# Performance work log

Hardware: AMD Instinct MI355X
Metric: run time of the kernel (lower is better)

The kernel has to match this reference:

```python
import jax, jax.numpy as jnp
import numpy as np

B, T, S, D, V, L = 32, 128, 256, 1024, 10000, 2
EOS = 2


def setup_inputs() -> dict:
    key = jax.random.key(0)
    ks = jax.random.split(key, 12)
    s = 0.02
    targets = jax.random.randint(ks[0], (B, T), 0, V)
    targets = jnp.where(targets == EOS, 3, targets)  # decoder strips eos; keep rectangular
    return {
        'encoder_outputs': jax.random.normal(ks[1], (B, S, D), jnp.float32),
        'targets': targets,
        'emb': jax.random.normal(ks[2], (V, D)) * s,
        'W_ih': jax.random.normal(ks[3], (L, 4 * D, D)) * s,
        'W_hh': jax.random.normal(ks[4], (L, 4 * D, D)) * s,
        'b_ih': jnp.zeros((L, 4 * D)),
        'b_hh': jnp.zeros((L, 4 * D)),
        'Wconv': jax.random.normal(ks[5], (D, 3)) * s,   # Conv1d(1 -> attn_dim, k=3) kernel
        'bconv': jnp.zeros((D,)),
        'Wq': jax.random.normal(ks[6], (D, D)) * s,      # query_proj (no bias)
        'Wv': jax.random.normal(ks[7], (D, D)) * s,      # value_proj (no bias)
        'attn_bias': jax.random.uniform(ks[8], (D,), minval=-0.1, maxval=0.1),
        'fc_attn_w': jax.random.normal(ks[9], (D,)) * s, # attention score fc (D -> 1)
        'fc_attn_b': jnp.zeros(()),
        'fc1_w': jax.random.normal(ks[10], (D, 2 * D)) * s,  # Linear(2D -> D)
        'fc1_b': jnp.zeros((D,)),
        'fc2_w': jax.random.normal(ks[11], (V, D)) * s,      # Linear(D -> V)
        'fc2_b': jnp.zeros((V,)),
    }


def _forward(encoder_outputs, targets, emb, W_ih, W_hh, b_ih, b_hh, Wconv, bconv,
             Wq, Wv, attn_bias, fc_attn_w, fc_attn_b, fc1_w, fc1_b, fc2_w, fc2_b):
    b, s_len = encoder_outputs.shape[0], encoder_outputs.shape[1]
    # value_proj(encoder_outputs) is constant across decode steps
    vproj = jnp.einsum('bsd,ed->bse', encoder_outputs, Wv)
    embedded = emb[targets]                  # (B,T,D)
    xs = jnp.swapaxes(embedded, 0, 1)        # (T,B,D)
    h0 = jnp.zeros((L, b, D), embedded.dtype)
    c0 = jnp.zeros((L, b, D), embedded.dtype)
    a0 = jnp.zeros((b, s_len), embedded.dtype)  # last alignment energy starts at zero

    def step(carry, x_t):
        h, c, attn = carry
        inp = x_t
        hs, cs = [], []
        for l in range(L):  # fixed small number of LSTM layers
            gates = inp @ W_ih[l].T + b_ih[l] + h[l] @ W_hh[l].T + b_hh[l]
            i, f, g, o = jnp.split(gates, 4, axis=-1)
            c_l = jax.nn.sigmoid(f) * c[l] + jax.nn.sigmoid(i) * jnp.tanh(g)
            h_l = jax.nn.sigmoid(o) * jnp.tanh(c_l)
            hs.append(h_l); cs.append(c_l); inp = h_l
        q = inp  # decoder rnn output for this step, (B,D)
        # location_conv: Conv1d(1->D, k=3, pad=1) over last alignment
        pad = jnp.pad(attn, ((0, 0), (1, 1)))
        win = jnp.stack([pad[:, :-2], pad[:, 1:-1], pad[:, 2:]], axis=-1)  # (B,S,3)
        loc = jnp.einsum('bsk,dk->bsd', win, Wconv) + bconv
        qp = q @ Wq.T
        e = jnp.tanh(qp[:, None, :] + vproj + loc + attn_bias)  # (B,S,D)
        energy = jnp.einsum('bsd,d->bs', e, fc_attn_w) + fc_attn_b
        new_attn = jax.nn.softmax(energy, axis=-1)
        context = jnp.einsum('bs,bsd->bd', new_attn, encoder_outputs)
        hid = jnp.tanh(jnp.concatenate([q, context], axis=-1) @ fc1_w.T + fc1_b)
        logp = jax.nn.log_softmax(hid @ fc2_w.T + fc2_b, axis=-1)
        return (jnp.stack(hs), jnp.stack(cs), new_attn), logp

    _, logps = jax.lax.scan(step, (h0, c0, a0), xs)  # (T,B,V)
    return jnp.swapaxes(logps, 0, 1)                 # (B,T,V) log-probs


def reference(encoder_outputs, targets, emb, W_ih, W_hh, b_ih, b_hh, Wconv, bconv,
              Wq, Wv, attn_bias, fc_attn_w, fc_attn_b, fc1_w, fc1_b, fc2_w, fc2_b):
    return _forward(encoder_outputs, targets, emb, W_ih, W_hh, b_ih, b_hh, Wconv, bconv,
                    Wq, Wv, attn_bias, fc_attn_w, fc_attn_b, fc1_w, fc1_b, fc2_w, fc2_b)
```

## Files before the change

kernel.cpp:

```cpp
#include <hip/hip_runtime.h>
#include <stdint.h>

#define B_ 32
#define T_ 128
#define S_ 256
#define D_ 1024
#define V_ 10000

typedef unsigned short u16;
typedef unsigned long long u64;
typedef __attribute__((ext_vector_type(8))) short bf16x8;
typedef __attribute__((ext_vector_type(4))) float f32x4;

__device__ __forceinline__ float bf2f(u16 u){ union { unsigned int i; float f; } v; v.i = ((unsigned int)u)<<16; return v.f; }
__device__ __forceinline__ u16 f2bf(float f){ union { float ff; unsigned int i; } v; v.ff = f; unsigned int x = v.i; return (u16)((x + 0x7fffu + ((x>>16)&1u))>>16); }
__device__ __forceinline__ float ftanh(float x){
  float e = __expf(2.f*x);
  return __builtin_fmaf(-2.f, __builtin_amdgcn_rcpf(1.f+e), 1.f);
}
__device__ __forceinline__ float sigm(float x){
  return __builtin_amdgcn_rcpf(1.f + __expf(-x));
}

__global__ void k_cast(const float* __restrict__ in, u16* __restrict__ out, long n){
  for (long i = (long)blockIdx.x*blockDim.x + threadIdx.x; i < n; i += (long)gridDim.x*blockDim.x)
    out[i] = f2bf(in[i]);
}

__global__ void k_w1cat(const float* __restrict__ wih1, const float* __restrict__ whh1, u16* __restrict__ out){
  const long n = (long)4096*2048;
  for (long i = (long)blockIdx.x*blockDim.x + threadIdx.x; i < n; i += (long)gridDim.x*blockDim.x){
    int row = (int)(i >> 11), k = (int)(i & 2047);
    float v = (k < D_) ? wih1[(size_t)row*D_ + k] : whh1[(size_t)row*D_ + (k - D_)];
    out[i] = f2bf(v);
  }
}

__global__ void k_bias(const float* __restrict__ bih, const float* __restrict__ bhh,
                       const float* __restrict__ bcv, const float* __restrict__ abias,
                       const float* __restrict__ Wcv, const float* __restrict__ fcw,
                       float* __restrict__ bias0, float* __restrict__ bias1,
                       float* __restrict__ biasE, float* __restrict__ convw){
  int i = blockIdx.x*blockDim.x + threadIdx.x;
  if (i < 4096){ bias0[i] = bih[i]+bhh[i]; bias1[i] = bih[4096+i]+bhh[4096+i]; }
  if (i < 1024){
    biasE[i] = bcv[i]+abias[i];
    convw[i*4+0]=Wcv[i*3+0]; convw[i*4+1]=Wcv[i*3+1]; convw[i*4+2]=Wcv[i*3+2]; convw[i*4+3]=fcw[i];
  }
}

__global__ void k_gather(const float* __restrict__ emb, const int* __restrict__ tgt, u16* __restrict__ embA){
  int row = blockIdx.x;
  int t = row >> 5, b = row & 31;
  int e = tgt[b*T_ + t];
  const float* src = emb + (size_t)e*D_;
  u16* dst = embA + (size_t)row*D_;
  for (int d = threadIdx.x; d < D_; d += 256) dst[d] = f2bf(src[d]);
}

__device__ __forceinline__ void gld_lds(const u16* g, u16* l){
  __builtin_amdgcn_global_load_lds((const __attribute__((address_space(1))) unsigned int*)g,
                                   (__attribute__((address_space(3))) unsigned int*)l, 16, 0, 0);
}

template<int OUT_MODE, bool SWIZ>
__global__ __launch_bounds__(256) void k_gemm128(const u16* __restrict__ Am, const u16* __restrict__ Bm,
      const float* __restrict__ bias, void* __restrict__ Cout, int M, int N, int K, int lda, int ldc)
{
  __shared__ u16 As[128*32];
  __shared__ u16 Bs[128*32];
  int bm = blockIdx.y*128, bn = blockIdx.x*128;
  int tid = threadIdx.x;
  int wv = tid>>6, lane = tid&63;
  int wm = (wv>>1)*64, wn = (wv&1)*64;
  int r = lane&15, kh = lane>>4;
  f32x4 zero = {0.f,0.f,0.f,0.f};
  f32x4 acc[4][4];
  #pragma unroll
  for (int mi=0;mi<4;mi++)
    #pragma unroll
    for (int ni=0;ni<4;ni++) acc[mi][ni] = zero;

  for (int k0 = 0; k0 < K; k0 += 32){
    #pragma unroll
    for (int i=0;i<2;i++){
      int c = tid + i*256;
      int row = c>>2, ko = (c&3)*8;
      int ga = bm+row; if (ga > M-1) ga = M-1;
      gld_lds(Am + (size_t)ga*lda + k0 + ko, As + c*8);
      int gb = bn+row; if (gb > N-1) gb = N-1;
      gld_lds(Bm + (size_t)gb*K + k0 + ko, Bs + c*8);
    }
    __syncthreads();
    bf16x8 af[4], bfv[4];
    #pragma unroll
    for (int mi=0;mi<4;mi++) af[mi]  = *(const bf16x8*)(As + (wm+mi*16+r)*32 + kh*8);
    #pragma unroll
    for (int ni=0;ni<4;ni++) bfv[ni] = *(const bf16x8*)(Bs + (wn+ni*16+r)*32 + kh*8);
    #pragma unroll
    for (int mi=0;mi<4;mi++)
      #pragma unroll
      for (int ni=0;ni<4;ni++)
        acc[mi][ni] = __builtin_amdgcn_mfma_f32_16x16x32_bf16(af[mi], bfv[ni], acc[mi][ni], 0,0,0);
    __syncthreads();
  }
  #pragma unroll
  for (int mi=0;mi<4;mi++)
    #pragma unroll
    for (int ni=0;ni<4;ni++)
      #pragma unroll
      for (int rr=0;rr<4;rr++){
        int grow = bm+wm+mi*16+kh*4+rr;
        int gcol = bn+wn+ni*16+r;
        if (grow < M && gcol < N){
          float v = acc[mi][ni][rr];
          if (bias) v += bias[gcol];
          size_t orow = SWIZ ? (size_t)((grow&31)*T_ + (grow>>5)) : (size_t)grow;
          if (OUT_MODE==0)      ((float*)Cout)[orow*(size_t)ldc + gcol] = v;
          else if (OUT_MODE==1) ((u16*)Cout)[orow*(size_t)ldc + gcol] = f2bf(v);
          else                  ((u16*)Cout)[orow*(size_t)ldc + gcol] = f2bf(ftanh(v));
        }
      }
}

__device__ __forceinline__ void xcd_barrier(int* barL, int it){
  asm volatile("s_waitcnt vmcnt(0)" ::: "memory");
  __syncthreads();
  if (threadIdx.x==0){
    int grp = blockIdx.x & 7;
    int* gcnt = barL + grp*32;
    int* root = barL + 256;
    int* rel  = barL + 320 + grp*32;
    int v = __hip_atomic_fetch_add(gcnt, 1, __ATOMIC_RELAXED, __HIP_MEMORY_SCOPE_AGENT);
    if (v == 32*(it+1) - 1){
      int rv = __hip_atomic_fetch_add(root, 1, __ATOMIC_RELAXED, __HIP_MEMORY_SCOPE_AGENT);
      if (rv == 8*(it+1) - 1){
        #pragma unroll
        for (int g2=0; g2<8; ++g2)
          __hip_atomic_store(barL + 320 + g2*32, it+1, __ATOMIC_RELAXED, __HIP_MEMORY_SCOPE_AGENT);
      }
    }
    while (__hip_atomic_load(rel, __ATOMIC_RELAXED, __HIP_MEMORY_SCOPE_AGENT) < it+1)
      __builtin_amdgcn_s_sleep(8);
  }
  __syncthreads();
}

__device__ __forceinline__ void ring_barrier(int* cnt, int nblk, int it){
  asm volatile("s_waitcnt vmcnt(0)" ::: "memory");
  __syncthreads();
  if (threadIdx.x==0){
    __hip_atomic_fetch_add(cnt, 1, __ATOMIC_RELAXED, __HIP_MEMORY_SCOPE_AGENT);
    int target = nblk*(it+1);
    while (__hip_atomic_load(cnt, __ATOMIC_RELAXED, __HIP_MEMORY_SCOPE_AGENT) < target)
      __builtin_amdgcn_s_sleep(4);
  }
  __syncthreads();
}

__global__ __launch_bounds__(512) void k_lstm_p(const u16* __restrict__ Whh0, const u16* __restrict__ W1cat,
    const u16* __restrict__ X0, const float* __restrict__ bias1,
    u16* __restrict__ Hh, u16* __restrict__ qcat, int* __restrict__ barL)
{
  __shared__ u16 W0s[16*1024];
  __shared__ u16 W1s[16*2048];
  __shared__ float gl0[8*512];
  __shared__ float gl1[8*512];
  __shared__ u16 hb0[128];
  __shared__ u16 hb1[128];
  int bid = blockIdx.x, tid = threadIdx.x;
  int w = tid>>6, lane = tid&63, r = lane&15, kh = lane>>4;
  for (int ci = tid; ci < 2048; ci += 512){
    int row = ci>>7, c = ci&127;
    int grow = (row>>2)*1024 + bid*4 + (row&3);
    bf16x8 v = *(const bf16x8*)(Whh0 + (size_t)grow*1024 + c*8);
    *(bf16x8*)(W0s + (size_t)(((row<<7) + (c ^ (row&7)))*8)) = v;
  }
  for (int ci = tid; ci < 4096; ci += 512){
    int row = ci>>8, c = ci&255;
    int grow = (row>>2)*1024 + bid*4 + (row&3);
    bf16x8 v = *(const bf16x8*)(W1cat + (size_t)grow*2048 + c*8);
    *(bf16x8*)(W1s + (size_t)(((row<<8) + (c ^ (row&7)))*8)) = v;
  }
  __syncthreads();
  float c0reg = 0.f, c1reg = 0.f;
  int cb = tid>>2, cj = tid&3;
  int col = bid*4 + cj;
  float b1i=0.f, b1f=0.f, b1g=0.f, b1o=0.f;
  if (tid < 128){ b1i=bias1[col]; b1f=bias1[1024+col]; b1g=bias1[2048+col]; b1o=bias1[3072+col]; }
  for (int p = 0; p <= T_; ++p){
    const u16* Hprev = Hh + (size_t)p*65536;
    u16* Hcur = (u16*)Hh + (size_t)(p+1)*65536;
    bool doG0 = (p < T_), doG1 = (p > 0);
    float x_gi=0.f, x_gf=0.f, x_gg=0.f, x_go=0.f;
    if (doG0 && tid < 128){
      const u16* xr = X0 + ((size_t)p*32 + cb)*4096 + col;
      x_gi = bf2f(xr[0]); x_gf = bf2f(xr[1024]); x_gg = bf2f(xr[2048]); x_go = bf2f(xr[3072]);
    }
    f32x4 acc00={0.f,0.f,0.f,0.f}, acc01={0.f,0.f,0.f,0.f};
    f32x4 acc10={0.f,0.f,0.f,0.f}, acc11={0.f,0.f,0.f,0.f};
    bf16x8 a_g0[2][4], a_g1[2][8];
    if (doG0){
      const u16* a0 = Hprev + (size_t)r*2048 + w*128 + kh*8;
      const u16* a1 = Hprev + (size_t)(16+r)*2048 + w*128 + kh*8;
      #pragma unroll
      for (int kk=0;kk<4;kk++){ a_g0[0][kk] = *(const bf16x8*)(a0 + kk*32);
                                a_g0[1][kk] = *(const bf16x8*)(a1 + kk*32); }
    }
    if (doG1){
      const u16* a0 = Hprev + (size_t)r*2048 + w*256 + kh*8;
      const u16* a1 = Hprev + (size_t)(16+r)*2048 + w*256 + kh*8;
      #pragma unroll
      for (int kk=0;kk<8;kk++){ a_g1[0][kk] = *(const bf16x8*)(a0 + kk*32);
                                a_g1[1][kk] = *(const bf16x8*)(a1 + kk*32); }
    }
    if (doG0){
      #pragma unroll
      for (int kk=0;kk<4;kk++){
        int c = (w<<4) + (kk<<2) + kh;
        bf16x8 bv = *(const bf16x8*)(W0s + (size_t)((((int)r<<7) + (c ^ (r&7)))*8));
        acc00 = __builtin_amdgcn_mfma_f32_16x16x32_bf16(a_g0[0][kk], bv, acc00, 0,0,0);
        acc01 = __builtin_amdgcn_mfma_f32_16x16x32_bf16(a_g0[1][kk], bv, acc01, 0,0,0);
      }
    }
    if (doG1){
      #pragma unroll
      for (int kk=0;kk<8;kk++){
        int c = (w<<5) + (kk<<2) + kh;
        bf16x8 bv = *(const bf16x8*)(W1s + (size_t)((((int)r<<8) + (c ^ (r&7)))*8));
        acc10 = __builtin_amdgcn_mfma_f32_16x16x32_bf16(a_g1[0][kk], bv, acc10, 0,0,0);
        acc11 = __builtin_amdgcn_mfma_f32_16x16x32_bf16(a_g1[1][kk], bv, acc11, 0,0,0);
      }
    }
    #pragma unroll
    for (int rr=0;rr<4;rr++){
      gl0[w*512 + (kh*4+rr)*16 + r]    = acc00[rr];
      gl0[w*512 + (16+kh*4+rr)*16 + r] = acc01[rr];
      gl1[w*512 + (kh*4+rr)*16 + r]    = acc10[rr];
      gl1[w*512 + (16+kh*4+rr)*16 + r] = acc11[rr];
    }
    __syncthreads();
    if (tid < 128){
      if (doG0){
        float gi=x_gi, gf=x_gf, gg=x_gg, go=x_go;
        #pragma unroll
        for (int ww=0;ww<8;ww++){
          const float* gp = gl0 + ww*512 + cb*16 + cj;
          gi += gp[0]; gf += gp[4]; gg += gp[8]; go += gp[12];
        }
        float cn = sigm(gf)*c0reg + sigm(gi)*ftanh(gg);
        float hn = sigm(go)*ftanh(cn); c0reg = cn;
        hb0[tid] = f2bf(hn);
      }
      if (doG1){
        float gi=b1i, gf=b1f, gg=b1g, go=b1o;
        #pragma unroll
        for (int ww=0;ww<8;ww++){
          const float* gp = gl1 + ww*512 + cb*16 + cj;
          gi += gp[0]; gf += gp[4]; gg += gp[8]; go += gp[12];
        }
        float cn = sigm(gf)*c1reg + sigm(gi)*ftanh(gg);
        float hn = sigm(go)*ftanh(cn); c1reg = cn;
        hb1[tid] = f2bf(hn);
      }
    }
    __syncthreads();
    if (tid < 32){
      union { u64 v; u16 s[4]; } pk;
      if (doG0){
        pk.s[0]=hb0[tid*4]; pk.s[1]=hb0[tid*4+1]; pk.s[2]=hb0[tid*4+2]; pk.s[3]=hb0[tid*4+3];
        __hip_atomic_store((u64*)(Hcur + (size_t)tid*2048 + bid*4), pk.v,
                           __ATOMIC_RELAXED, __HIP_MEMORY_SCOPE_AGENT);
      }
      if (doG1){
        pk.s[0]=hb1[tid*4]; pk.s[1]=hb1[tid*4+1]; pk.s[2]=hb1[tid*4+2]; pk.s[3]=hb1[tid*4+3];
        __hip_atomic_store((u64*)(Hcur + (size_t)tid*2048 + 1024 + bid*4), pk.v,
                           __ATOMIC_RELAXED, __HIP_MEMORY_SCOPE_AGENT);
        *(u64*)(qcat + ((size_t)(p-1)*32 + tid)*2048 + bid*4) = pk.v;
      }
    }
    if (p < T_) xcd_barrier(barL, p);
  }
}

__global__ __launch_bounds__(512) void k_attn_p(const u16* __restrict__ vpb, const u16* __restrict__ qpb,
    const u16* __restrict__ enc, const float* __restrict__ convw,
    float* __restrict__ eng, u16* __restrict__ qcat, int* __restrict__ barA)
{
  __shared__ float aw[256];
  __shared__ float red[16];
  __shared__ float cred[512];
  int bid = blockIdx.x, tid = threadIdx.x;
  int b = bid>>3, p = bid&7;
  int w = tid>>6, lane = tid&63;
  int d0 = lane*16;
  f32x4 cw[16];
  #pragma unroll
  for (int j=0;j<16;j++) cw[j] = *(const f32x4*)(convw + (size_t)(d0+j)*4);
  if (tid < 256) aw[tid] = 0.f;
  __syncthreads();
  int* cnt = barA + b*32;
  for (int t=0; t<T_; ++t){
    float* ebuf = eng + (t&1)*8192 + b*256;
    const u16* qrow = qpb + ((size_t)t*32 + b)*1024 + d0;
    bf16x8 q0 = *(const bf16x8*)qrow, q1 = *(const bf16x8*)(qrow+8);
    float qf[16];
    #pragma unroll
    for (int j=0;j<16;j++) qf[j] = bf2f((u16)(j<8 ? q0[j] : q1[j-8]));
    #pragma unroll
    for (int ss=0; ss<4; ++ss){
      int s = p*32 + w*4 + ss;
      float am = (s>0)   ? aw[s-1] : 0.f;
      float ac =           aw[s];
      float ap = (s<255) ? aw[s+1] : 0.f;
      const u16* vrow = vpb + ((size_t)(b*256+s))*1024 + d0;
      bf16x8 v0 = *(const bf16x8*)vrow, v1 = *(const bf16x8*)(vrow+8);
      float sum = 0.f;
      #pragma unroll
      for (int j=0;j<16;j++){
        float vv = bf2f((u16)(j<8 ? v0[j] : v1[j-8]));
        float x = qf[j] + vv + am*cw[j][0] + ac*cw[j][1] + ap*cw[j][2];
        sum += ftanh(x)*cw[j][3];
      }
      #pragma unroll
      for (int o=32;o;o>>=1) sum += __shfl_xor(sum, o);
      if (lane==0)
        __hip_atomic_store(ebuf + s, sum, __ATOMIC_RELAXED, __HIP_MEMORY_SCOPE_AGENT);
    }
    ring_barrier(cnt, 8, t);
    float e_val = -3.0e38f;
    if (tid < 256)
      e_val = __hip_atomic_load(ebuf + tid, __ATOMIC_RELAXED, __HIP_MEMORY_SCOPE_AGENT);
    float m = e_val;
    #pragma unroll
    for (int o=32;o;o>>=1) m = fmaxf(m, __shfl_xor(m,o));
    if (lane==0) red[w] = m;
    __syncthreads();
    float mx = red[0];
    #pragma unroll
    for (int i2=1;i2<8;i2++) mx = fmaxf(mx, red[i2]);
    float ex = (tid < 256) ? __expf(e_val - mx) : 0.f;
    float sl = ex;
    #pragma unroll
    for (int o=32;o;o>>=1) sl += __shfl_xor(sl,o);
    __syncthreads();
    if (lane==0) red[8+w] = sl;
    __syncthreads();
    float st = red[8]+red[9]+red[10]+red[11]+red[12]+red[13]+red[14]+red[15];
    if (tid < 256) aw[tid] = ex * __builtin_amdgcn_rcpf(st);
    __syncthreads();
    int sq = tid>>7, dt = tid&127;
    const u16* ep = enc + (size_t)(b*256 + sq*64)*1024 + p*128 + dt;
    float a0=0.f,a1=0.f,a2=0.f,a3=0.f;
    #pragma unroll 4
    for (int s2=0;s2<64;s2+=4){
      a0 += aw[sq*64+s2]   * bf2f(ep[(size_t)(s2)  *1024]);
      a1 += aw[sq*64+s2+1] * bf2f(ep[(size_t)(s2+1)*1024]);
      a2 += aw[sq*64+s2+2] * bf2f(ep[(size_t)(s2+2)*1024]);
      a3 += aw[sq*64+s2+3] * bf2f(ep[(size_t)(s2+3)*1024]);
    }
    cred[tid] = a0+a1+a2+a3;
    __syncthreads();
    if (tid < 128)
      qcat[((size_t)t*32 + b)*2048 + 1024 + p*128 + tid] =
        f2bf(cred[tid]+cred[128+tid]+cred[256+tid]+cred[384+tid]);
    __syncthreads();
  }
}

__global__ __launch_bounds__(256) void k_logsm(float* __restrict__ out){
  int row = blockIdx.x, tid = threadIdx.x;
  float* p = out + (size_t)row*V_;
  __shared__ float red[4];
  float pv[40];
  int nv = 0;
  float mx = -3.0e38f;
  for (int v=tid; v<V_; v+=256){ float x = p[v]; pv[nv++] = x; mx = fmaxf(mx, x); }
  #pragma unroll
  for (int o=32;o;o>>=1) mx = fmaxf(mx, __shfl_xor(mx,o));
  if ((tid&63)==0) red[tid>>6]=mx;
  __syncthreads();
  mx = fmaxf(fmaxf(red[0],red[1]),fmaxf(red[2],red[3]));
  __syncthreads();
  float s = 0.f;
  for (int i=0;i<nv;i++) s += __expf(pv[i]-mx);
  #pragma unroll
  for (int o=32;o;o>>=1) s += __shfl_xor(s,o);
  if ((tid&63)==0) red[tid>>6]=s;
  __syncthreads();
  float lz = mx + __logf(red[0]+red[1]+red[2]+red[3]);
  { int i=0; for (int v=tid; v<V_; v+=256) p[v] = pv[i++] - lz; }
}

extern "C" void kernel_launch(void* const* d_in, const int* in_sizes, int n_in,
                              void* d_out, int out_size, void* d_ws, size_t ws_size,
                              hipStream_t stream)
{
  const float* enc   = (const float*)d_in[0];
  const int*   tgt   = (const int*)  d_in[1];
  const float* emb   = (const float*)d_in[2];
  const float* Wih   = (const float*)d_in[3];
  const float* Whh   = (const float*)d_in[4];
  const float* bih   = (const float*)d_in[5];
  const float* bhh   = (const float*)d_in[6];
  const float* Wcv   = (const float*)d_in[7];
  const float* bcv   = (const float*)d_in[8];
  const float* Wq    = (const float*)d_in[9];
  const float* Wvm   = (const float*)d_in[10];
  const float* abias = (const float*)d_in[11];
  const float* fcw   = (const float*)d_in[12];
  const float* fc1w  = (const float*)d_in[14];
  const float* fc1b  = (const float*)d_in[15];
  const float* fc2w  = (const float*)d_in[16];
  const float* fc2b  = (const float*)d_in[17];
  float* out = (float*)d_out;

  char* base = (char*)d_ws; size_t off = 0;
  auto A = [&](size_t nbytes)->char*{ char* q = base + off; off += (nbytes + 255) & ~(size_t)255; return q; };
  u16* enc_bf  = (u16*)A(8388608ull*2);
  u16* Wv_bf   = (u16*)A(1048576ull*2);
  u16* Wih0_bf = (u16*)A(4194304ull*2);
  u16* W1cat   = (u16*)A(8388608ull*2);
  u16* Whh0_bf = (u16*)A(4194304ull*2);
  u16* Wq_bf   = (u16*)A(1048576ull*2);
  u16* fc1w_bf = (u16*)A(2097152ull*2);
  u16* fc2w_bf = (u16*)A(10240000ull*2);
  u16* embA    = (u16*)A(4194304ull*2);
  u16* X0      = (u16*)A(16777216ull*2);
  u16* vpb     = (u16*)A(8388608ull*2);
  u16* qcat    = (u16*)A(8388608ull*2);
  float* bias0 = (float*)A(4096*4);
  float* bias1 = (float*)A(4096*4);
  float* biasE = (float*)A(1024*4);
  float* convw = (float*)A(4096*4);
  float* eng   = (float*)A(2*8192*4);
  int* barL    = (int*)A(4096);
  int* barA    = (int*)A(4096);
  u16* Hh      = fc2w_bf;
  u16* qpb     = embA;
  u16* hid     = embA;

  hipMemsetAsync(Hh, 0, 2*65536*2, stream);
  hipMemsetAsync(barL, 0, 4096, stream);
  hipMemsetAsync(barA, 0, 4096, stream);

  k_cast<<<2048,256,0,stream>>>(enc,  enc_bf,  8388608);
  k_cast<<<1024,256,0,stream>>>(Wih,  Wih0_bf, 4194304);
  k_cast<<<1024,256,0,stream>>>(Whh,  Whh0_bf, 4194304);
  k_cast<<<512,256,0,stream>>>(Wq,    Wq_bf,   1048576);
  k_cast<<<512,256,0,stream>>>(Wvm,   Wv_bf,   1048576);
  k_cast<<<512,256,0,stream>>>(fc1w,  fc1w_bf, 2097152);
  k_w1cat<<<2048,256,0,stream>>>(Wih + 4194304, Whh + 4194304, W1cat);
  k_bias<<<16,256,0,stream>>>(bih, bhh, bcv, abias, Wcv, fcw, bias0, bias1, biasE, convw);
  k_gather<<<4096,256,0,stream>>>(emb, tgt, embA);

  k_gemm128<1,false><<<dim3(8,64),256,0,stream>>>(enc_bf, Wv_bf, biasE, vpb, 8192, 1024, 1024, 1024, 1024);
  k_gemm128<1,false><<<dim3(32,32),256,0,stream>>>(embA, Wih0_bf, bias0, X0, 4096, 4096, 1024, 1024, 4096);

  {
    const u16* a0 = Whh0_bf; const u16* a1 = W1cat; const u16* a2 = X0; const float* a3 = bias1;
    u16* a4 = Hh; u16* a5 = qcat; int* a6 = barL;
    void* args[] = {(void*)&a0,(void*)&a1,(void*)&a2,(void*)&a3,(void*)&a4,(void*)&a5,(void*)&a6};
    hipError_t e = hipLaunchCooperativeKernel((const void*)k_lstm_p, dim3(256), dim3(512), args, 0, stream);
    if (e != hipSuccess)
      k_lstm_p<<<dim3(256),dim3(512),0,stream>>>(a0,a1,a2,a3,a4,a5,a6);
  }

  k_gemm128<1,false><<<dim3(8,32),256,0,stream>>>(qcat, Wq_bf, nullptr, qpb, 4096, 1024, 1024, 2048, 1024);

  {
    const u16* a0 = vpb; const u16* a1 = qpb; const u16* a2 = enc_bf; const float* a3 = convw;
    float* a4 = eng; u16* a5 = qcat; int* a6 = barA;
    void* args[] = {(void*)&a0,(void*)&a1,(void*)&a2,(void*)&a3,(void*)&a4,(void*)&a5,(void*)&a6};
    hipError_t e = hipLaunchCooperativeKernel((const void*)k_attn_p, dim3(256), dim3(512), args, 0, stream);
    if (e != hipSuccess)
      k_attn_p<<<dim3(256),dim3(512),0,stream>>>(a0,a1,a2,a3,a4,a5,a6);
  }

  k_gemm128<2,false><<<dim3(8,32),256,0,stream>>>(qcat, fc1w_bf, fc1b, hid, 4096, 1024, 2048, 2048, 1024);
  k_cast<<<2048,256,0,stream>>>(fc2w, fc2w_bf, 10240000);
  k_gemm128<0,true><<<dim3(79,32),256,0,stream>>>(hid, fc2w_bf, fc2b, out, 4096, V_, 1024, 1024, V_);
  k_logsm<<<4096,256,0,stream>>>(out);
}
```

Before: 2.791 ms.

## Fuse LSTM, query projection and attention into one pipelined persistent kernel

Merges the persistent LSTM kernel, the Wq query-projection GEMM and the persistent attention kernel into a single cooperative kernel. The query projection, energy computation and softmax/context stages are software-pipelined across loop iterations (offsets of 2, 3 and 4 steps behind the LSTM) and share one grid barrier per iteration. This removes two kernel launches and the separate attention kernel's serialized T-step loop with its own barriers, overlapping attention work with the LSTM recurrence. In exchange each iteration carries more work and LDS, and every block now pays the full grid barrier for attention steps that previously only needed an 8-block group barrier.

```diff
diff --git a/kernel.cpp b/kernel.cpp
--- a/kernel.cpp
+++ b/kernel.cpp
@@ -146,30 +146,28 @@
   __syncthreads();
 }
 
-__device__ __forceinline__ void ring_barrier(int* cnt, int nblk, int it){
-  asm volatile("s_waitcnt vmcnt(0)" ::: "memory");
-  __syncthreads();
-  if (threadIdx.x==0){
-    __hip_atomic_fetch_add(cnt, 1, __ATOMIC_RELAXED, __HIP_MEMORY_SCOPE_AGENT);
-    int target = nblk*(it+1);
-    while (__hip_atomic_load(cnt, __ATOMIC_RELAXED, __HIP_MEMORY_SCOPE_AGENT) < target)
-      __builtin_amdgcn_s_sleep(4);
-  }
-  __syncthreads();
-}
-
-__global__ __launch_bounds__(512) void k_lstm_p(const u16* __restrict__ Whh0, const u16* __restrict__ W1cat,
-    const u16* __restrict__ X0, const float* __restrict__ bias1,
-    u16* __restrict__ Hh, u16* __restrict__ qcat, int* __restrict__ barL)
+__global__ __launch_bounds__(512) void k_fused(const u16* __restrict__ Whh0, const u16* __restrict__ W1cat,
+    const u16* __restrict__ Wqm, const u16* __restrict__ X0, const float* __restrict__ bias1,
+    const u16* __restrict__ vpb, const u16* __restrict__ enc, const float* __restrict__ convw,
+    u16* __restrict__ Hh, u16* __restrict__ qps, float* __restrict__ eng,
+    u16* __restrict__ qcat, int* __restrict__ barL)
 {
   __shared__ u16 W0s[16*1024];
   __shared__ u16 W1s[16*2048];
+  __shared__ u16 Wqs[4*1024];
   __shared__ float gl0[8*512];
   __shared__ float gl1[8*512];
+  __shared__ float glq[4*128];
+  __shared__ float aw[256];
+  __shared__ float red[16];
+  __shared__ float cred[512];
   __shared__ u16 hb0[128];
   __shared__ u16 hb1[128];
+  __shared__ u16 hbq[128];
   int bid = blockIdx.x, tid = threadIdx.x;
   int w = tid>>6, lane = tid&63, r = lane&15, kh = lane>>4;
+  int batt = bid>>3, part = bid&7;
+  int d0 = lane*16;
   for (int ci = tid; ci < 2048; ci += 512){
     int row = ci>>7, c = ci&127;
     int grow = (row>>2)*1024 + bid*4 + (row&3);
@@ -182,23 +180,32 @@
     bf16x8 v = *(const bf16x8*)(W1cat + (size_t)grow*2048 + c*8);
     *(bf16x8*)(W1s + (size_t)(((row<<8) + (c ^ (row&7)))*8)) = v;
   }
+  {
+    int row = tid>>7, c = tid&127;
+    bf16x8 v = *(const bf16x8*)(Wqm + (size_t)(bid*4+row)*1024 + c*8);
+    *(bf16x8*)(Wqs + (size_t)(((row<<7) + (c ^ (row&7)))*8)) = v;
+  }
+  if (tid < 256) aw[tid] = 0.f;
   __syncthreads();
   float c0reg = 0.f, c1reg = 0.f;
   int cb = tid>>2, cj = tid&3;
   int col = bid*4 + cj;
   float b1i=0.f, b1f=0.f, b1g=0.f, b1o=0.f;
   if (tid < 128){ b1i=bias1[col]; b1f=bias1[1024+col]; b1g=bias1[2048+col]; b1o=bias1[3072+col]; }
-  for (int p = 0; p <= T_; ++p){
-    const u16* Hprev = Hh + (size_t)p*65536;
-    u16* Hcur = (u16*)Hh + (size_t)(p+1)*65536;
-    bool doG0 = (p < T_), doG1 = (p > 0);
+  for (int i = 0; i <= T_+3; ++i){
+    const u16* Hprev = Hh + (size_t)i*65536;
+    u16* Hcur = (u16*)Hh + (size_t)(i+1)*65536;
+    bool doG0 = (i < T_);
+    bool doG1 = (i >= 1 && i <= T_);
+    bool loadG1 = (i >= 1 && i <= T_+1);
+    bool doQP = (i >= 2 && i <= T_+1);
+    bool doEN = (i >= 3 && i <= T_+2);
+    bool doSM = (i >= 4);
     float x_gi=0.f, x_gf=0.f, x_gg=0.f, x_go=0.f;
     if (doG0 && tid < 128){
-      const u16* xr = X0 + ((size_t)p*32 + cb)*4096 + col;
+      const u16* xr = X0 + ((size_t)i*32 + cb)*4096 + col;
       x_gi = bf2f(xr[0]); x_gf = bf2f(xr[1024]); x_gg = bf2f(xr[2048]); x_go = bf2f(xr[3072]);
     }
-    f32x4 acc00={0.f,0.f,0.f,0.f}, acc01={0.f,0.f,0.f,0.f};
-    f32x4 acc10={0.f,0.f,0.f,0.f}, acc11={0.f,0.f,0.f,0.f};
     bf16x8 a_g0[2][4], a_g1[2][8];
     if (doG0){
       const u16* a0 = Hprev + (size_t)r*2048 + w*128 + kh*8;
@@ -207,13 +214,56 @@
       for (int kk=0;kk<4;kk++){ a_g0[0][kk] = *(const bf16x8*)(a0 + kk*32);
                                 a_g0[1][kk] = *(const bf16x8*)(a1 + kk*32); }
     }
-    if (doG1){
+    if (loadG1){
       const u16* a0 = Hprev + (size_t)r*2048 + w*256 + kh*8;
       const u16* a1 = Hprev + (size_t)(16+r)*2048 + w*256 + kh*8;
       #pragma unroll
       for (int kk=0;kk<8;kk++){ a_g1[0][kk] = *(const bf16x8*)(a0 + kk*32);
                                 a_g1[1][kk] = *(const bf16x8*)(a1 + kk*32); }
     }
+    if (doSM){
+      int t = i-4;
+      float* ebuf = eng + (t&1)*8192 + batt*256;
+      float e_val = -3.0e38f;
+      if (tid < 256)
+        e_val = __hip_atomic_load(ebuf + tid, __ATOMIC_RELAXED, __HIP_MEMORY_SCOPE_AGENT);
+      float m = e_val;
+      #pragma unroll
+      for (int o=32;o;o>>=1) m = fmaxf(m, __shfl_xor(m,o));
+      if (lane==0) red[w] = m;
+      __syncthreads();
+      float mx = red[0];
+      #pragma unroll
+      for (int i2=1;i2<8;i2++) mx = fmaxf(mx, red[i2]);
+      float ex = (tid < 256) ? __expf(e_val - mx) : 0.f;
+      float sl = ex;
+      #pragma unroll
+      for (int o=32;o;o>>=1) sl += __shfl_xor(sl,o);
+      __syncthreads();
+      if (lane==0) red[8+w] = sl;
+      __syncthreads();
+      float st = red[8]+red[9]+red[10]+red[11]+red[12]+red[13]+red[14]+red[15];
+      if (tid < 256) aw[tid] = ex * __builtin_amdgcn_rcpf(st);
+      __syncthreads();
+      int sq = tid>>7, dt = tid&127;
+      const u16* ep = enc + (size_t)(batt*256 + sq*64)*1024 + part*128 + dt;
+      float a0=0.f,a1=0.f,a2=0.f,a3=0.f;
+      #pragma unroll 4
+      for (int s2=0;s2<64;s2+=4){
+        a0 += aw[sq*64+s2]   * bf2f(ep[(size_t)(s2)  *1024]);
+        a1 += aw[sq*64+s2+1] * bf2f(ep[(size_t)(s2+1)*1024]);
+        a2 += aw[sq*64+s2+2] * bf2f(ep[(size_t)(s2+2)*1024]);
+        a3 += aw[sq*64+s2+3] * bf2f(ep[(size_t)(s2+3)*1024]);
+      }
+      cred[tid] = a0+a1+a2+a3;
+      __syncthreads();
+      if (tid < 128)
+        qcat[((size_t)t*32 + batt)*2048 + 1024 + part*128 + tid] =
+          f2bf(cred[tid]+cred[128+tid]+cred[256+tid]+cred[384+tid]);
+    }
+    f32x4 acc00={0.f,0.f,0.f,0.f}, acc01={0.f,0.f,0.f,0.f};
+    f32x4 acc10={0.f,0.f,0.f,0.f}, acc11={0.f,0.f,0.f,0.f};
+    f32x4 accq0={0.f,0.f,0.f,0.f}, accq1={0.f,0.f,0.f,0.f};
     if (doG0){
       #pragma unroll
       for (int kk=0;kk<4;kk++){
@@ -232,12 +282,29 @@
         acc11 = __builtin_amdgcn_mfma_f32_16x16x32_bf16(a_g1[1][kk], bv, acc11, 0,0,0);
       }
     }
+    if (doQP && w >= 4){
+      #pragma unroll
+      for (int kk=0;kk<8;kk++){
+        int c = ((w-4)<<5) + (kk<<2) + kh;
+        int qrw = r & 3;
+        bf16x8 bv = *(const bf16x8*)(Wqs + (size_t)(((qrw<<7) + (c ^ (qrw&7)))*8));
+        accq0 = __builtin_amdgcn_mfma_f32_16x16x32_bf16(a_g1[0][kk], bv, accq0, 0,0,0);
+        accq1 = __builtin_amdgcn_mfma_f32_16x16x32_bf16(a_g1[1][kk], bv, accq1, 0,0,0);
+      }
+    }
     #pragma unroll
     for (int rr=0;rr<4;rr++){
       gl0[w*512 + (kh*4+rr)*16 + r]    = acc00[rr];
       gl0[w*512 + (16+kh*4+rr)*16 + r] = acc01[rr];
       gl1[w*512 + (kh*4+rr)*16 + r]    = acc10[rr];
       gl1[w*512 + (16+kh*4+rr)*16 + r] = acc11[rr];
+    }
+    if (doQP && w >= 4 && r < 4){
+      #pragma unroll
+      for (int rr=0;rr<4;rr++){
+        glq[(w-4)*128 + (kh*4+rr)*4 + r]      = accq0[rr];
+        glq[(w-4)*128 + (16+kh*4+rr)*4 + r]   = accq1[rr];
+      }
     }
     __syncthreads();
     if (tid < 128){
@@ -263,6 +330,8 @@
         float hn = sigm(go)*ftanh(cn); c1reg = cn;
         hb1[tid] = f2bf(hn);
       }
+      if (doQP)
+        hbq[tid] = f2bf(glq[tid] + glq[128+tid] + glq[256+tid] + glq[384+tid]);
     }
     __syncthreads();
     if (tid < 32){
@@ -276,95 +345,47 @@
         pk.s[0]=hb1[tid*4]; pk.s[1]=hb1[tid*4+1]; pk.s[2]=hb1[tid*4+2]; pk.s[3]=hb1[tid*4+3];
         __hip_atomic_store((u64*)(Hcur + (size_t)tid*2048 + 1024 + bid*4), pk.v,
                            __ATOMIC_RELAXED, __HIP_MEMORY_SCOPE_AGENT);
-        *(u64*)(qcat + ((size_t)(p-1)*32 + tid)*2048 + bid*4) = pk.v;
-      }
-    }
-    if (p < T_) xcd_barrier(barL, p);
-  }
-}
-
-__global__ __launch_bounds__(512) void k_attn_p(const u16* __restrict__ vpb, const u16* __restrict__ qpb,
-    const u16* __restrict__ enc, const float* __restrict__ convw,
-    float* __restrict__ eng, u16* __restrict__ qcat, int* __restrict__ barA)
-{
-  __shared__ float aw[256];
-  __shared__ float red[16];
-  __shared__ float cred[512];
-  int bid = blockIdx.x, tid = threadIdx.x;
-  int b = bid>>3, p = bid&7;
-  int w = tid>>6, lane = tid&63;
-  int d0 = lane*16;
-  f32x4 cw[16];
-  #pragma unroll
-  for (int j=0;j<16;j++) cw[j] = *(const f32x4*)(convw + (size_t)(d0+j)*4);
-  if (tid < 256) aw[tid] = 0.f;
-  __syncthreads();
-  int* cnt = barA + b*32;
-  for (int t=0; t<T_; ++t){
-    float* ebuf = eng + (t&1)*8192 + b*256;
-    const u16* qrow = qpb + ((size_t)t*32 + b)*1024 + d0;
-    bf16x8 q0 = *(const bf16x8*)qrow, q1 = *(const bf16x8*)(qrow+8);
-    float qf[16];
-    #pragma unroll
-    for (int j=0;j<16;j++) qf[j] = bf2f((u16)(j<8 ? q0[j] : q1[j-8]));
-    #pragma unroll
-    for (int ss=0; ss<4; ++ss){
-      int s = p*32 + w*4 + ss;
-      float am = (s>0)   ? aw[s-1] : 0.f;
-      float ac =           aw[s];
-      float ap = (s<255) ? aw[s+1] : 0.f;
-      const u16* vrow = vpb + ((size_t)(b*256+s))*1024 + d0;
-      bf16x8 v0 = *(const bf16x8*)vrow, v1 = *(const bf16x8*)(vrow+8);
-      float sum = 0.f;
-      #pragma unroll
-      for (int j=0;j<16;j++){
-        float vv = bf2f((u16)(j<8 ? v0[j] : v1[j-8]));
-        float x = qf[j] + vv + am*cw[j][0] + ac*cw[j][1] + ap*cw[j][2];
-        sum += ftanh(x)*cw[j][3];
-      }
-      #pragma unroll
-      for (int o=32;o;o>>=1) sum += __shfl_xor(sum, o);
-      if (lane==0)
-        __hip_atomic_store(ebuf + s, sum, __ATOMIC_RELAXED, __HIP_MEMORY_SCOPE_AGENT);
-    }
-    ring_barrier(cnt, 8, t);
-    float e_val = -3.0e38f;
-    if (tid < 256)
-      e_val = __hip_atomic_load(ebuf + tid, __ATOMIC_RELAXED, __HIP_MEMORY_SCOPE_AGENT);
-    float m = e_val;
-    #pragma unroll
-    for (int o=32;o;o>>=1) m = fmaxf(m, __shfl_xor(m,o));
-    if (lane==0) red[w] = m;
-    __syncthreads();
-    float mx = red[0];
-    #pragma unroll
-    for (int i2=1;i2<8;i2++) mx = fmaxf(mx, red[i2]);
-    float ex = (tid < 256) ? __expf(e_val - mx) : 0.f;
-    float sl = ex;
-    #pragma unroll
-    for (int o=32;o;o>>=1) sl += __shfl_xor(sl,o);
-    __syncthreads();
-    if (lane==0) red[8+w] = sl;
-    __syncthreads();
-    float st = red[8]+red[9]+red[10]+red[11]+red[12]+red[13]+red[14]+red[15];
-    if (tid < 256) aw[tid] = ex * __builtin_amdgcn_rcpf(st);
-    __syncthreads();
-    int sq = tid>>7, dt = tid&127;
-    const u16* ep = enc + (size_t)(b*256 + sq*64)*1024 + p*128 + dt;
-    float a0=0.f,a1=0.f,a2=0.f,a3=0.f;
-    #pragma unroll 4
-    for (int s2=0;s2<64;s2+=4){
-      a0 += aw[sq*64+s2]   * bf2f(ep[(size_t)(s2)  *1024]);
-      a1 += aw[sq*64+s2+1] * bf2f(ep[(size_t)(s2+1)*1024]);
-      a2 += aw[sq*64+s2+2] * bf2f(ep[(size_t)(s2+2)*1024]);
-      a3 += aw[sq*64+s2+3] * bf2f(ep[(size_t)(s2+3)*1024]);
-    }
-    cred[tid] = a0+a1+a2+a3;
-    __syncthreads();
-    if (tid < 128)
-      qcat[((size_t)t*32 + b)*2048 + 1024 + p*128 + tid] =
-        f2bf(cred[tid]+cred[128+tid]+cred[256+tid]+cred[384+tid]);
-    __syncthreads();
+        *(u64*)(qcat + ((size_t)(i-1)*32 + tid)*2048 + bid*4) = pk.v;
+      }
+      if (doQP){
+        pk.s[0]=hbq[tid*4]; pk.s[1]=hbq[tid*4+1]; pk.s[2]=hbq[tid*4+2]; pk.s[3]=hbq[tid*4+3];
+        __hip_atomic_store((u64*)(qps + ((size_t)(i-2)*32 + tid)*1024 + bid*4), pk.v,
+                           __ATOMIC_RELAXED, __HIP_MEMORY_SCOPE_AGENT);
+      }
+    }
+    if (doEN){
+      int t = i-3;
+      float* ebuf = eng + (t&1)*8192 + batt*256;
+      const u16* qrow = qps + ((size_t)t*32 + batt)*1024 + d0;
+      bf16x8 q0 = *(const bf16x8*)qrow, q1 = *(const bf16x8*)(qrow+8);
+      float qf[16];
+      #pragma unroll
+      for (int j=0;j<16;j++) qf[j] = bf2f((u16)(j<8 ? q0[j] : q1[j-8]));
+      f32x4 cw[16];
+      #pragma unroll
+      for (int j=0;j<16;j++) cw[j] = *(const f32x4*)(convw + (size_t)(d0+j)*4);
+      #pragma unroll
+      for (int ss=0; ss<4; ++ss){
+        int s = part*32 + w*4 + ss;
+        float am = (s>0)   ? aw[s-1] : 0.f;
+        float ac =           aw[s];
+        float av = (s<255) ? aw[s+1] : 0.f;
+        const u16* vrow = vpb + ((size_t)(batt*256+s))*1024 + d0;
+        bf16x8 v0 = *(const bf16x8*)vrow, v1 = *(const bf16x8*)(vrow+8);
+        float sum = 0.f;
+        #pragma unroll
+        for (int j=0;j<16;j++){
+          float vv = bf2f((u16)(j<8 ? v0[j] : v1[j-8]));
+          float x = qf[j] + vv + am*cw[j][0] + ac*cw[j][1] + av*cw[j][2];
+          sum += ftanh(x)*cw[j][3];
+        }
+        #pragma unroll
+        for (int o=32;o;o>>=1) sum += __shfl_xor(sum, o);
+        if (lane==0)
+          __hip_atomic_store(ebuf + s, sum, __ATOMIC_RELAXED, __HIP_MEMORY_SCOPE_AGENT);
+      }
+    }
+    if (i < T_+3) xcd_barrier(barL, i);
   }
 }
 
@@ -429,20 +450,18 @@
   u16* X0      = (u16*)A(16777216ull*2);
   u16* vpb     = (u16*)A(8388608ull*2);
   u16* qcat    = (u16*)A(8388608ull*2);
+  u16* qps     = (u16*)A(4194304ull*2);
   float* bias0 = (float*)A(4096*4);
   float* bias1 = (float*)A(4096*4);
   float* biasE = (float*)A(1024*4);
   float* convw = (float*)A(4096*4);
   float* eng   = (float*)A(2*8192*4);
   int* barL    = (int*)A(4096);
-  int* barA    = (int*)A(4096);
   u16* Hh      = fc2w_bf;
-  u16* qpb     = embA;
   u16* hid     = embA;
 
   hipMemsetAsync(Hh, 0, 2*65536*2, stream);
   hipMemsetAsync(barL, 0, 4096, stream);
-  hipMemsetAsync(barA, 0, 4096, stream);
 
   k_cast<<<2048,256,0,stream>>>(enc,  enc_bf,  8388608);
   k_cast<<<1024,256,0,stream>>>(Wih,  Wih0_bf, 4194304);
@@ -458,23 +477,14 @@
   k_gemm128<1,false><<<dim3(32,32),256,0,stream>>>(embA, Wih0_bf, bias0, X0, 4096, 4096, 1024, 1024, 4096);
 
   {
-    const u16* a0 = Whh0_bf; const u16* a1 = W1cat; const u16* a2 = X0; const float* a3 = bias1;
-    u16* a4 = Hh; u16* a5 = qcat; int* a6 = barL;
-    void* args[] = {(void*)&a0,(void*)&a1,(void*)&a2,(void*)&a3,(void*)&a4,(void*)&a5,(void*)&a6};
-    hipError_t e = hipLaunchCooperativeKernel((const void*)k_lstm_p, dim3(256), dim3(512), args, 0, stream);
+    const u16* a0 = Whh0_bf; const u16* a1 = W1cat; const u16* a2 = Wq_bf; const u16* a3 = X0;
+    const float* a4 = bias1; const u16* a5 = vpb; const u16* a6 = enc_bf; const float* a7 = convw;
+    u16* a8 = Hh; u16* a9 = qps; float* a10 = eng; u16* a11 = qcat; int* a12 = barL;
+    void* args[] = {(void*)&a0,(void*)&a1,(void*)&a2,(void*)&a3,(void*)&a4,(void*)&a5,(void*)&a6,
+                    (void*)&a7,(void*)&a8,(void*)&a9,(void*)&a10,(void*)&a11,(void*)&a12};
+    hipError_t e = hipLaunchCooperativeKernel((const void*)k_fused, dim3(256), dim3(512), args, 0, stream);
     if (e != hipSuccess)
-      k_lstm_p<<<dim3(256),dim3(512),0,stream>>>(a0,a1,a2,a3,a4,a5,a6);
-  }
-
-  k_gemm128<1,false><<<dim3(8,32),256,0,stream>>>(qcat, Wq_bf, nullptr, qpb, 4096, 1024, 1024, 2048, 1024);
-
-  {
-    const u16* a0 = vpb; const u16* a1 = qpb; const u16* a2 = enc_bf; const float* a3 = convw;
-    float* a4 = eng; u16* a5 = qcat; int* a6 = barA;
-    void* args[] = {(void*)&a0,(void*)&a1,(void*)&a2,(void*)&a3,(void*)&a4,(void*)&a5,(void*)&a6};
-    hipError_t e = hipLaunchCooperativeKernel((const void*)k_attn_p, dim3(256), dim3(512), args, 0, stream);
-    if (e != hipSuccess)
-      k_attn_p<<<dim3(256),dim3(512),0,stream>>>(a0,a1,a2,a3,a4,a5,a6);
+      k_fused<<<dim3(256),dim3(512),0,stream>>>(a0,a1,a2,a3,a4,a5,a6,a7,a8,a9,a10,a11,a12);
   }
 
   k_gemm128<2,false><<<dim3(8,32),256,0,stream>>>(qcat, fc1w_bf, fc1b, hid, 4096, 1024, 2048, 2048, 1024);
```

Result: slower. 3.667 ms (+31.4%).

## Fuse query projection into persistent LSTM kernel using idle warps

Applied to the files above, without the earlier changes.

Removes the separate q @ Wq GEMM launch by computing the query projection inside the persistent LSTM kernel. Each block keeps its 4 rows of Wq in shared memory and uses warps 4-7 to multiply the layer-1 hidden state loaded for the next step. This adds one extra recurrence iteration, and one more grid barrier, to drain the last projection. It also adds per-step MFMA work and shared-memory traffic to the latency-critical recurrent loop.

```diff
diff --git a/kernel.cpp b/kernel.cpp
--- a/kernel.cpp
+++ b/kernel.cpp
@@ -159,13 +159,15 @@
 }
 
 __global__ __launch_bounds__(512) void k_lstm_p(const u16* __restrict__ Whh0, const u16* __restrict__ W1cat,
-    const u16* __restrict__ X0, const float* __restrict__ bias1,
-    u16* __restrict__ Hh, u16* __restrict__ qcat, int* __restrict__ barL)
+    const u16* __restrict__ Wqm, const u16* __restrict__ X0, const float* __restrict__ bias1,
+    u16* __restrict__ Hh, u16* __restrict__ qcat, u16* __restrict__ qps, int* __restrict__ barL)
 {
   __shared__ u16 W0s[16*1024];
   __shared__ u16 W1s[16*2048];
+  __shared__ u16 Wqs[4*1024];
   __shared__ float gl0[8*512];
   __shared__ float gl1[8*512];
+  __shared__ float glq[4*128];
   __shared__ u16 hb0[128];
   __shared__ u16 hb1[128];
   int bid = blockIdx.x, tid = threadIdx.x;
@@ -182,16 +184,24 @@
     bf16x8 v = *(const bf16x8*)(W1cat + (size_t)grow*2048 + c*8);
     *(bf16x8*)(W1s + (size_t)(((row<<8) + (c ^ (row&7)))*8)) = v;
   }
+  {
+    int row = tid>>7, c = tid&127;
+    bf16x8 v = *(const bf16x8*)(Wqm + (size_t)(bid*4+row)*1024 + c*8);
+    *(bf16x8*)(Wqs + (size_t)(((row<<7) + (c ^ (row&7)))*8)) = v;
+  }
   __syncthreads();
   float c0reg = 0.f, c1reg = 0.f;
   int cb = tid>>2, cj = tid&3;
   int col = bid*4 + cj;
   float b1i=0.f, b1f=0.f, b1g=0.f, b1o=0.f;
   if (tid < 128){ b1i=bias1[col]; b1f=bias1[1024+col]; b1g=bias1[2048+col]; b1o=bias1[3072+col]; }
-  for (int p = 0; p <= T_; ++p){
+  for (int p = 0; p <= T_+1; ++p){
     const u16* Hprev = Hh + (size_t)p*65536;
     u16* Hcur = (u16*)Hh + (size_t)(p+1)*65536;
-    bool doG0 = (p < T_), doG1 = (p > 0);
+    bool doG0 = (p < T_);
+    bool doG1 = (p >= 1 && p <= T_);
+    bool loadG1 = (p >= 1);
+    bool doQP = (p >= 2);
     float x_gi=0.f, x_gf=0.f, x_gg=0.f, x_go=0.f;
     if (doG0 && tid < 128){
       const u16* xr = X0 + ((size_t)p*32 + cb)*4096 + col;
@@ -199,6 +209,7 @@
     }
     f32x4 acc00={0.f,0.f,0.f,0.f}, acc01={0.f,0.f,0.f,0.f};
     f32x4 acc10={0.f,0.f,0.f,0.f}, acc11={0.f,0.f,0.f,0.f};
+    f32x4 accq0={0.f,0.f,0.f,0.f}, accq1={0.f,0.f,0.f,0.f};
     bf16x8 a_g0[2][4], a_g1[2][8];
     if (doG0){
       const u16* a0 = Hprev + (size_t)r*2048 + w*128 + kh*8;
@@ -207,7 +218,7 @@
       for (int kk=0;kk<4;kk++){ a_g0[0][kk] = *(const bf16x8*)(a0 + kk*32);
                                 a_g0[1][kk] = *(const bf16x8*)(a1 + kk*32); }
     }
-    if (doG1){
+    if (loadG1){
       const u16* a0 = Hprev + (size_t)r*2048 + w*256 + kh*8;
       const u16* a1 = Hprev + (size_t)(16+r)*2048 + w*256 + kh*8;
       #pragma unroll
@@ -232,12 +243,29 @@
         acc11 = __builtin_amdgcn_mfma_f32_16x16x32_bf16(a_g1[1][kk], bv, acc11, 0,0,0);
       }
     }
+    if (doQP && w >= 4){
+      #pragma unroll
+      for (int kk=0;kk<8;kk++){
+        int c = ((w-4)<<5) + (kk<<2) + kh;
+        int qrw = r & 3;
+        bf16x8 bv = *(const bf16x8*)(Wqs + (size_t)(((qrw<<7) + (c ^ (qrw&7)))*8));
+        accq0 = __builtin_amdgcn_mfma_f32_16x16x32_bf16(a_g1[0][kk], bv, accq0, 0,0,0);
+        accq1 = __builtin_amdgcn_mfma_f32_16x16x32_bf16(a_g1[1][kk], bv, accq1, 0,0,0);
+      }
+    }
     #pragma unroll
     for (int rr=0;rr<4;rr++){
       gl0[w*512 + (kh*4+rr)*16 + r]    = acc00[rr];
       gl0[w*512 + (16+kh*4+rr)*16 + r] = acc01[rr];
       gl1[w*512 + (kh*4+rr)*16 + r]    = acc10[rr];
       gl1[w*512 + (16+kh*4+rr)*16 + r] = acc11[rr];
+    }
+    if (doQP && w >= 4 && r < 4){
+      #pragma unroll
+      for (int rr=0;rr<4;rr++){
+        glq[(w-4)*128 + (kh*4+rr)*4 + r]    = accq0[rr];
+        glq[(w-4)*128 + (16+kh*4+rr)*4 + r] = accq1[rr];
+      }
     }
     __syncthreads();
     if (tid < 128){
@@ -263,6 +291,10 @@
         float hn = sigm(go)*ftanh(cn); c1reg = cn;
         hb1[tid] = f2bf(hn);
       }
+      if (doQP){
+        float hq = glq[cb*4+cj] + glq[128 + cb*4+cj] + glq[256 + cb*4+cj] + glq[384 + cb*4+cj];
+        qps[((size_t)(p-2)*32 + cb)*1024 + col] = f2bf(hq);
+      }
     }
     __syncthreads();
     if (tid < 32){
@@ -279,7 +311,7 @@
         *(u64*)(qcat + ((size_t)(p-1)*32 + tid)*2048 + bid*4) = pk.v;
       }
     }
-    if (p < T_) xcd_barrier(barL, p);
+    if (p < T_+1) xcd_barrier(barL, p);
   }
 }
 
@@ -437,7 +469,7 @@
   int* barL    = (int*)A(4096);
   int* barA    = (int*)A(4096);
   u16* Hh      = fc2w_bf;
-  u16* qpb     = embA;
+  u16* qps     = embA;
   u16* hid     = embA;
 
   hipMemsetAsync(Hh, 0, 2*65536*2, stream);
@@ -458,18 +490,17 @@
   k_gemm128<1,false><<<dim3(32,32),256,0,stream>>>(embA, Wih0_bf, bias0, X0, 4096, 4096, 1024, 1024, 4096);
 
   {
-    const u16* a0 = Whh0_bf; const u16* a1 = W1cat; const u16* a2 = X0; const float* a3 = bias1;
-    u16* a4 = Hh; u16* a5 = qcat; int* a6 = barL;
-    void* args[] = {(void*)&a0,(void*)&a1,(void*)&a2,(void*)&a3,(void*)&a4,(void*)&a5,(void*)&a6};
+    const u16* a0 = Whh0_bf; const u16* a1 = W1cat; const u16* a2 = Wq_bf; const u16* a3 = X0;
+    const float* a4 = bias1; u16* a5 = Hh; u16* a6 = qcat; u16* a7 = qps; int* a8 = barL;
+    void* args[] = {(void*)&a0,(void*)&a1,(void*)&a2,(void*)&a3,(void*)&a4,(void*)&a5,
+                    (void*)&a6,(void*)&a7,(void*)&a8};
     hipError_t e = hipLaunchCooperativeKernel((const void*)k_lstm_p, dim3(256), dim3(512), args, 0, stream);
     if (e != hipSuccess)
-      k_lstm_p<<<dim3(256),dim3(512),0,stream>>>(a0,a1,a2,a3,a4,a5,a6);
-  }
-
-  k_gemm128<1,false><<<dim3(8,32),256,0,stream>>>(qcat, Wq_bf, nullptr, qpb, 4096, 1024, 1024, 2048, 1024);
+      k_lstm_p<<<dim3(256),dim3(512),0,stream>>>(a0,a1,a2,a3,a4,a5,a6,a7,a8);
+  }
 
   {
-    const u16* a0 = vpb; const u16* a1 = qpb; const u16* a2 = enc_bf; const float* a3 = convw;
+    const u16* a0 = vpb; const u16* a1 = qps; const u16* a2 = enc_bf; const float* a3 = convw;
     float* a4 = eng; u16* a5 = qcat; int* a6 = barA;
     void* args[] = {(void*)&a0,(void*)&a1,(void*)&a2,(void*)&a3,(void*)&a4,(void*)&a5,(void*)&a6};
     hipError_t e = hipLaunchCooperativeKernel((const void*)k_attn_p, dim3(256), dim3(512), args, 0, stream);
```

Measured after the change: 2.809 ms. About the same (+0.6%).
